# Kernel optimization log

Hardware: AMD Instinct MI355X
Metric: run time of the kernel (lower is better)

## Reference

```python
import jax, jax.numpy as jnp
import numpy as np

BETA = 0.25

def setup_inputs() -> dict:
    key = jax.random.key(0)
    k1, k2 = jax.random.split(key)
    x = jax.random.normal(k1, (32, 1024, 256), dtype=jnp.float32)
    # tf.random_uniform_initializer default range is [-0.05, 0.05)
    embedding = jax.random.uniform(k2, (256, 8192), dtype=jnp.float32, minval=-0.05, maxval=0.05)
    return {"x": x, "embedding": embedding}


def reference(x, embedding):
    # x: [B, S, D]; embedding: [D, K] (codebook stored column-wise, as in the tf module)
    D = x.shape[-1]
    flat = x.reshape(-1, D)                                   # [N, D]
    dists = (jnp.sum(flat * flat, axis=1, keepdims=True)
             - 2.0 * (flat @ embedding)
             + jnp.sum(embedding * embedding, axis=0))
    idx = jnp.argmin(dists, axis=1)                           # [N] int
    quantized = jnp.take(embedding.T, idx, axis=0).reshape(x.shape)  # gather codebook columns
    # VQ losses
    commitment = jnp.mean(jnp.square(jax.lax.stop_gradient(quantized) - x))
    codebook = jnp.mean(jnp.square(quantized - jax.lax.stop_gradient(x)))
    loss = BETA * commitment + codebook
    # straight-through estimator
    quantized_st = x + jax.lax.stop_gradient(quantized - x)
    return quantized_st, loss
```

## Files before the change

kernel.cpp:

```cpp
#include <hip/hip_runtime.h>

typedef float f4   __attribute__((ext_vector_type(4)));
typedef float f2   __attribute__((ext_vector_type(2)));
typedef _Float16 f16x8 __attribute__((ext_vector_type(8)));
typedef float f32x4  __attribute__((ext_vector_type(4)));

#define N_ROWS  32768
#define D_DIM   256
#define K_CODES 8192
#define NUM_ELEM (N_ROWS * D_DIM)
#define EPS_MARGIN 2e-3f
#define FB_CAP  8192
#define FB_RPB  8
#define RF_SLICES 16
#define N_PANELS 256
#define QTR_PANELS 64

__device__ __forceinline__ void gl2lds16(const void* g, void* l) {
    __builtin_amdgcn_global_load_lds(
        (const __attribute__((address_space(1))) unsigned int*)g,
        (__attribute__((address_space(3))) unsigned int*)l, 16, 0, 0);
}

__global__ void ee_kernel(const float* __restrict__ E, float* __restrict__ ee) {
    const int k = blockIdx.x * blockDim.x + threadIdx.x;
    double s = 0.0;
    for (int d = 0; d < D_DIM; ++d) {
        float v = E[(size_t)d * K_CODES + k];
        s += (double)v * (double)v;
    }
    ee[k] = (float)s;
}

__global__ void prep_kernel(const float* __restrict__ E, short* __restrict__ Ep) {
    const int p  = blockIdx.x;
    const int t  = threadIdx.x;
    const int c  = t & 31;
    const int gq = t >> 5;
    const int cp = p * 32;
    short* ph = Ep + (size_t)p * 8192;
    #pragma unroll
    for (int gi = 0; gi < 4; ++gi) {
        int g = gq * 4 + gi;
        f16x8 h;
        #pragma unroll
        for (int j = 0; j < 8; ++j) {
            float v = E[(size_t)(g * 8 + j) * K_CODES + cp + c];
            h[j] = (_Float16)v;
        }
        *(f16x8*)(ph + (g * 32 + c) * 8) = h;
    }
}

__global__ void trans32_kernel(const float* __restrict__ E, float* __restrict__ Et32) {
    __shared__ float tile[64][65];
    const int t  = threadIdx.x;
    const int k0 = blockIdx.x * 64, d0 = blockIdx.y * 64;
    #pragma unroll
    for (int i = 0; i < 16; ++i) {
        int dd = i * 4 + (t >> 6), kk = t & 63;
        tile[dd][kk] = E[(size_t)(d0 + dd) * K_CODES + k0 + kk];
    }
    __syncthreads();
    #pragma unroll
    for (int i = 0; i < 16; ++i) {
        int kk = i * 4 + (t >> 6), dd = t & 63;
        Et32[(size_t)(k0 + kk) * D_DIM + d0 + dd] = tile[dd][kk];
    }
}

__launch_bounds__(256, 4)
__global__ void mfma_sieve_kernel(const float* __restrict__ X,
                                  const short* __restrict__ Ep,
                                  const float* __restrict__ ee,
                                  f2* __restrict__ res_bs,
                                  int* __restrict__ res_idx) {
    __shared__ __align__(16) short Bbuf[2][8192];
    __shared__ float eebuf[2048];
    const int t    = threadIdx.x;
    const int w    = t >> 6;
    const int lane = t & 63;
    const int n    = lane & 15;
    const int quad = lane >> 4;
    const int part = blockIdx.x & 3;
    const int row0 = (blockIdx.x >> 2) * 128;
    const int rw   = row0 + w * 32;
    const int p0   = part * QTR_PANELS;

    f16x8 Ah[2][8];
    #pragma unroll
    for (int rt = 0; rt < 2; ++rt) {
        const float* xp = X + (size_t)(rw + rt * 16 + n) * D_DIM;
        #pragma unroll
        for (int ks = 0; ks < 8; ++ks) {
            int d = ks * 32 + quad * 8;
            f4 a = *(const f4*)(xp + d);
            f4 b = *(const f4*)(xp + d + 4);
            f16x8 h;
            #pragma unroll
            for (int j = 0; j < 8; ++j) {
                float x = (j < 4) ? a[j] : b[j - 4];
                h[j] = (_Float16)x;
            }
            Ah[rt][ks] = h;
        }
    }

    {
        const f4* src = (const f4*)(ee + part * 2048);
        f4* dst = (f4*)eebuf;
        dst[t * 2]     = src[t * 2];
        dst[t * 2 + 1] = src[t * 2 + 1];
    }

    float bestv[8], secv[8]; int besti[8];
    #pragma unroll
    for (int s = 0; s < 8; ++s) { bestv[s] = -1e30f; secv[s] = -1e30f; besti[s] = 0; }

    {
        const char* gp = (const char*)Ep + (size_t)p0 * 16384;
        char* lp = (char*)&Bbuf[0][0];
        #pragma unroll
        for (int i = 0; i < 4; ++i)
            gl2lds16(gp + (w * 4 + i) * 1024 + lane * 16, lp + (w * 4 + i) * 1024);
    }
    __syncthreads();

    for (int i = 0; i < QTR_PANELS; ++i) {
        const int p   = p0 + i;
        const int buf = i & 1;
        if (i + 1 < QTR_PANELS) {
            const char* gp = (const char*)Ep + (size_t)(p + 1) * 16384;
            char* lp = (char*)&Bbuf[buf ^ 1][0];
            #pragma unroll
            for (int k = 0; k < 4; ++k)
                gl2lds16(gp + (w * 4 + k) * 1024 + lane * 16, lp + (w * 4 + k) * 1024);
        }

        const short* Bh = &Bbuf[buf][0];
        const int po = i * 32;

        float eh0 = -0.5f * eebuf[po + n];
        float eh1 = -0.5f * eebuf[po + 16 + n];
        f32x4 acc[2][2];
        #pragma unroll
        for (int rt = 0; rt < 2; ++rt) {
            #pragma unroll
            for (int r = 0; r < 4; ++r) { acc[0][rt][r] = eh0; acc[1][rt][r] = eh1; }
        }

        #pragma unroll
        for (int ks = 0; ks < 8; ++ks) {
            const int g = ks * 4 + quad;
            f16x8 bh[2];
            #pragma unroll
            for (int ct = 0; ct < 2; ++ct) {
                int c = ct * 16 + n;
                bh[ct] = *(const f16x8*)(Bh + (g * 32 + c) * 8);
            }
            #pragma unroll
            for (int ct = 0; ct < 2; ++ct)
                #pragma unroll
                for (int rt = 0; rt < 2; ++rt)
                    acc[ct][rt] = __builtin_amdgcn_mfma_f32_16x16x32_f16(Ah[rt][ks], bh[ct], acc[ct][rt], 0, 0, 0);
        }

        const int cb = p * 32;
        #pragma unroll
        for (int ct = 0; ct < 2; ++ct) {
            int code = cb + ct * 16 + n;
            #pragma unroll
            for (int rt = 0; rt < 2; ++rt)
                #pragma unroll
                for (int r = 0; r < 4; ++r) {
                    float av = acc[ct][rt][r];
                    int s = rt * 4 + r;
                    float nb = fmaxf(av, bestv[s]);
                    secv[s]  = fmaxf(secv[s], fminf(av, bestv[s]));
                    besti[s] = (av > bestv[s]) ? code : besti[s];
                    bestv[s] = nb;
                }
        }
        __syncthreads();
    }

    #pragma unroll
    for (int off = 1; off < 16; off <<= 1) {
        #pragma unroll
        for (int s = 0; s < 8; ++s) {
            float ov = __shfl_xor(bestv[s], off);
            int   oi = __shfl_xor(besti[s], off);
            float os = __shfl_xor(secv[s], off);
            bool owin = (ov > bestv[s]) || (ov == bestv[s] && oi < besti[s]);
            if (owin) { secv[s] = fmaxf(os, bestv[s]); bestv[s] = ov; besti[s] = oi; }
            else      { secv[s] = fmaxf(secv[s], ov); }
        }
    }

    if (n == 0) {
        #pragma unroll
        for (int s = 0; s < 8; ++s) {
            int rl  = w * 32 + (s >> 2) * 16 + quad * 4 + (s & 3);
            int row = row0 + rl;
            f2 bs; bs[0] = -2.0f * bestv[s]; bs[1] = -2.0f * secv[s];
            res_bs[(size_t)row * 4 + part]  = bs;
            res_idx[(size_t)row * 4 + part] = besti[s];
        }
    }
}

__global__ void merge_kernel(const f2* __restrict__ res_bs, const int* __restrict__ res_idx,
                             int* __restrict__ bidx, int* __restrict__ counter,
                             int2* __restrict__ list) {
    const int row = blockIdx.x * blockDim.x + threadIdx.x;
    if (row >= N_ROWS) return;
    float gb = 1e30f, gs = 1e30f; int gi = 0;
    #pragma unroll
    for (int p = 0; p < 4; ++p) {
        f2 v  = res_bs[(size_t)row * 4 + p];
        int vi = res_idx[(size_t)row * 4 + p];
        if (v[0] < gb) { gs = fminf(gb, v[1]); gb = v[0]; gi = vi; }
        else           { gs = fminf(gs, v[0]); }
    }
    bidx[row] = gi;
    if (gs - gb <= EPS_MARGIN) {
        int pos = atomicAdd(counter, 1);
        if (pos < FB_CAP) list[pos] = make_int2(row, gi);
    }
}

__global__ void gather_kernel(const float* __restrict__ X, const float* __restrict__ Et32,
                              const int* __restrict__ bidx, float* __restrict__ out,
                              double* __restrict__ loss_sum) {
    __shared__ int bl_[128];
    const int t    = threadIdx.x;
    const int row0 = blockIdx.x * 128;
    if (t < 128) bl_[t] = bidx[row0 + t];
    __syncthreads();
    double ls = 0.0;
    const int d = t;
    #pragma unroll 4
    for (int r = 0; r < 128; ++r) {
        int code = bl_[r];
        float q  = Et32[(size_t)code * D_DIM + d];
        float x  = X[(size_t)(row0 + r) * D_DIM + d];
        float dq = q - x;
        out[(size_t)(row0 + r) * D_DIM + d] = x + dq;
        ls += (double)dq * (double)dq;
    }
    #pragma unroll
    for (int off = 32; off > 0; off >>= 1)
        ls += __shfl_down(ls, off);
    if ((t & 63) == 0) atomicAdd(loss_sum, ls);
}

__global__ void refine1_kernel(const float* __restrict__ X, const float* __restrict__ E,
                               const int* __restrict__ counter, const int2* __restrict__ list,
                               double* __restrict__ res_v, int* __restrict__ res_i) {
    __shared__ float xt[D_DIM][FB_RPB];
    __shared__ int rows_sh[FB_RPB];
    __shared__ double wbv[4][FB_RPB];
    __shared__ int    wbi[4][FB_RPB];

    int nf = *counter; if (nf > FB_CAP) nf = FB_CAP;
    const int nchunks = (nf + FB_RPB - 1) / FB_RPB;
    const int nitems  = nchunks * RF_SLICES;
    const int t = threadIdx.x;

    for (int item = blockIdx.x; item < nitems; item += gridDim.x) {
        const int rc = item / RF_SLICES;
        const int sl = item % RF_SLICES;
        __syncthreads();
        if (t < FB_RPB) {
            int e = rc * FB_RPB + t;
            int2 ent = list[(e < nf) ? e : 0];
            rows_sh[t] = ent.x;
        }
        __syncthreads();
        #pragma unroll
        for (int j = 0; j < FB_RPB; ++j)
            xt[t][j] = X[(size_t)rows_sh[j] * D_DIM + t];
        __syncthreads();

        const int k0 = sl * 512 + t * 2;
        double s0[FB_RPB], s1[FB_RPB], q0 = 0.0, q1 = 0.0;
        #pragma unroll
        for (int j = 0; j < FB_RPB; ++j) { s0[j] = 0.0; s1[j] = 0.0; }
        for (int d = 0; d < D_DIM; ++d) {
            f2 ev = *(const f2*)(E + (size_t)d * K_CODES + k0);
            double e0d = (double)ev[0], e1d = (double)ev[1];
            const f4* xp = (const f4*)(&xt[d][0]);
            f4 xa = xp[0], xb = xp[1];
            double xd[FB_RPB] = { (double)xa[0], (double)xa[1], (double)xa[2], (double)xa[3],
                                  (double)xb[0], (double)xb[1], (double)xb[2], (double)xb[3] };
            q0 += e0d * e0d; q1 += e1d * e1d;
            #pragma unroll
            for (int j = 0; j < FB_RPB; ++j) {
                s0[j] += xd[j] * e0d;
                s1[j] += xd[j] * e1d;
            }
        }
        double bv[FB_RPB]; int bi[FB_RPB];
        #pragma unroll
        for (int j = 0; j < FB_RPB; ++j) {
            double k0v = q0 - 2.0 * s0[j];
            double k1v = q1 - 2.0 * s1[j];
            bv[j] = k0v; bi[j] = k0;
            if (k1v < bv[j]) { bv[j] = k1v; bi[j] = k0 + 1; }
        }
        #pragma unroll
        for (int off = 1; off < 64; off <<= 1) {
            #pragma unroll
            for (int j = 0; j < FB_RPB; ++j) {
                double ov = __shfl_xor(bv[j], off);
                int    oi = __shfl_xor(bi[j], off);
                if (ov < bv[j] || (ov == bv[j] && oi < bi[j])) { bv[j] = ov; bi[j] = oi; }
            }
        }
        const int wave = t >> 6;
        if ((t & 63) == 0) {
            #pragma unroll
            for (int j = 0; j < FB_RPB; ++j) { wbv[wave][j] = bv[j]; wbi[wave][j] = bi[j]; }
        }
        __syncthreads();
        if (t < FB_RPB) {
            double b = wbv[0][t]; int i_ = wbi[0][t];
            #pragma unroll
            for (int wv = 1; wv < 4; ++wv) {
                double ov = wbv[wv][t]; int oi = wbi[wv][t];
                if (ov < b || (ov == b && oi < i_)) { b = ov; i_ = oi; }
            }
            int e = rc * FB_RPB + t;
            res_v[(size_t)e * RF_SLICES + sl] = b;
            res_i[(size_t)e * RF_SLICES + sl] = i_;
        }
    }
}

__global__ void patch_kernel(const float* __restrict__ X, const float* __restrict__ Et32,
                             float* __restrict__ out, double* __restrict__ loss_sum,
                             const int* __restrict__ counter, const int2* __restrict__ list,
                             const double* __restrict__ res_v, const int* __restrict__ res_i) {
    int nf = *counter; if (nf > FB_CAP) nf = FB_CAP;
    const int b = blockIdx.x;
    if (b >= nf) return;
    __shared__ int nc_sh;
    const int t = threadIdx.x;
    if (t == 0) {
        double bv = res_v[(size_t)b * RF_SLICES]; int bi = res_i[(size_t)b * RF_SLICES];
        for (int s = 1; s < RF_SLICES; ++s) {
            double v = res_v[(size_t)b * RF_SLICES + s];
            int    i = res_i[(size_t)b * RF_SLICES + s];
            if (v < bv || (v == bv && i < bi)) { bv = v; bi = i; }
        }
        nc_sh = bi;
    }
    __syncthreads();
    int2 ent = list[b];
    const int oc = ent.y, row = ent.x, nc = nc_sh;
    if (nc == oc) return;
    float x  = X[(size_t)row * D_DIM + t];
    float qn = Et32[(size_t)nc * D_DIM + t];
    float qo = Et32[(size_t)oc * D_DIM + t];
    float dqn = qn - x, dqo = qo - x;
    out[(size_t)row * D_DIM + t] = x + dqn;
    double dl = (double)dqn * dqn - (double)dqo * dqo;
    #pragma unroll
    for (int off = 32; off > 0; off >>= 1)
        dl += __shfl_down(dl, off);
    if ((t & 63) == 0) atomicAdd(loss_sum, dl);
}

__global__ void fin_kernel(const double* __restrict__ loss_sum, float* __restrict__ out) {
    double m = loss_sum[0] / (double)NUM_ELEM;
    out[NUM_ELEM] = (float)(0.25 * m + m);
}

extern "C" void kernel_launch(void* const* d_in, const int* in_sizes, int n_in,
                              void* d_out, int out_size, void* d_ws, size_t ws_size,
                              hipStream_t stream) {
    const float* X = (const float*)d_in[0];
    const float* E = (const float*)d_in[1];
    float* out = (float*)d_out;

    double* loss_sum = (double*)d_ws;
    int*    counter  = (int*)((char*)d_ws + 8);
    float*  ee       = (float*)((char*)d_ws + 1024);
    int2*   list     = (int2*)((char*)d_ws + 36864);
    double* res_v    = (double*)((char*)d_ws + 131072);
    int*    res_i    = (int*)((char*)d_ws + 1179648);
    float*  Et32     = (float*)((char*)d_ws + 1703936);
    short*  Ep       = (short*)((char*)d_ws + 10092544);
    f2*     res_bs   = (f2*)((char*)d_ws + 14286848);
    int*    res_idx  = (int*)((char*)d_ws + 15335424);
    int*    bidx     = (int*)((char*)d_ws + 19267584);

    hipMemsetAsync(d_ws, 0, 1024, stream);
    prep_kernel<<<N_PANELS, 256, 0, stream>>>(E, Ep);
    trans32_kernel<<<dim3(128, 4), 256, 0, stream>>>(E, Et32);
    ee_kernel<<<K_CODES / 256, 256, 0, stream>>>(E, ee);
    mfma_sieve_kernel<<<1024, 256, 0, stream>>>(X, Ep, ee, res_bs, res_idx);
    merge_kernel<<<N_ROWS / 256, 256, 0, stream>>>(res_bs, res_idx, bidx, counter, list);
    gather_kernel<<<N_ROWS / 128, 256, 0, stream>>>(X, Et32, bidx, out, loss_sum);
    refine1_kernel<<<2048, 256, 0, stream>>>(X, E, counter, list, res_v, res_i);
    patch_kernel<<<FB_CAP, 256, 0, stream>>>(X, Et32, out, loss_sum, counter, list,
                                             res_v, res_i);
    fin_kernel<<<1, 1, 0, stream>>>(loss_sum, out);
}
```

Baseline: 365.3 us.

## Fuse codebook prep kernels and fold merge into gather kernel

Combines the fp16 panel packing, fp32 transpose and codebook norm computation into one prep kernel that reads E once. The per-row merge of partial argmin results moves into the gather kernel, so the separate merge launch and the bidx buffer go away. The norm now accumulates in fp32 instead of fp64, which could slightly change near-tie decisions. The sieve kernel's launch-bounds occupancy hint also drops from 4 to 2 blocks per CU, which gives it more registers but lowers occupancy.

```diff
diff --git a/kernel.cpp b/kernel.cpp
--- a/kernel.cpp
+++ b/kernel.cpp
@@ -22,54 +22,43 @@
         (__attribute__((address_space(3))) unsigned int*)l, 16, 0, 0);
 }
 
-__global__ void ee_kernel(const float* __restrict__ E, float* __restrict__ ee) {
-    const int k = blockIdx.x * blockDim.x + threadIdx.x;
-    double s = 0.0;
-    for (int d = 0; d < D_DIM; ++d) {
-        float v = E[(size_t)d * K_CODES + k];
-        s += (double)v * (double)v;
-    }
-    ee[k] = (float)s;
-}
-
-__global__ void prep_kernel(const float* __restrict__ E, short* __restrict__ Ep) {
+__global__ void prep_kernel(const float* __restrict__ E, short* __restrict__ Ep,
+                            float* __restrict__ Et32, float* __restrict__ ee) {
+    __shared__ float eepart[8][32];
     const int p  = blockIdx.x;
     const int t  = threadIdx.x;
     const int c  = t & 31;
     const int gq = t >> 5;
     const int cp = p * 32;
     short* ph = Ep + (size_t)p * 8192;
+    float ss = 0.0f;
     #pragma unroll
     for (int gi = 0; gi < 4; ++gi) {
         int g = gq * 4 + gi;
         f16x8 h;
+        f4 av, bv;
         #pragma unroll
         for (int j = 0; j < 8; ++j) {
             float v = E[(size_t)(g * 8 + j) * K_CODES + cp + c];
             h[j] = (_Float16)v;
+            ss += v * v;
+            if (j < 4) av[j] = v; else bv[j - 4] = v;
         }
         *(f16x8*)(ph + (g * 32 + c) * 8) = h;
-    }
-}
-
-__global__ void trans32_kernel(const float* __restrict__ E, float* __restrict__ Et32) {
-    __shared__ float tile[64][65];
-    const int t  = threadIdx.x;
-    const int k0 = blockIdx.x * 64, d0 = blockIdx.y * 64;
-    #pragma unroll
-    for (int i = 0; i < 16; ++i) {
-        int dd = i * 4 + (t >> 6), kk = t & 63;
-        tile[dd][kk] = E[(size_t)(d0 + dd) * K_CODES + k0 + kk];
-    }
+        *(f4*)(Et32 + (size_t)(cp + c) * D_DIM + g * 8)     = av;
+        *(f4*)(Et32 + (size_t)(cp + c) * D_DIM + g * 8 + 4) = bv;
+    }
+    eepart[gq][c] = ss;
     __syncthreads();
-    #pragma unroll
-    for (int i = 0; i < 16; ++i) {
-        int kk = i * 4 + (t >> 6), dd = t & 63;
-        Et32[(size_t)(k0 + kk) * D_DIM + d0 + dd] = tile[dd][kk];
-    }
-}
-
-__launch_bounds__(256, 4)
+    if (t < 32) {
+        float s = 0.0f;
+        #pragma unroll
+        for (int q = 0; q < 8; ++q) s += eepart[q][t];
+        ee[cp + t] = s;
+    }
+}
+
+__launch_bounds__(256, 2)
 __global__ void mfma_sieve_kernel(const float* __restrict__ X,
                                   const short* __restrict__ Ep,
                                   const float* __restrict__ ee,
@@ -209,33 +198,29 @@
     }
 }
 
-__global__ void merge_kernel(const f2* __restrict__ res_bs, const int* __restrict__ res_idx,
-                             int* __restrict__ bidx, int* __restrict__ counter,
-                             int2* __restrict__ list) {
-    const int row = blockIdx.x * blockDim.x + threadIdx.x;
-    if (row >= N_ROWS) return;
-    float gb = 1e30f, gs = 1e30f; int gi = 0;
-    #pragma unroll
-    for (int p = 0; p < 4; ++p) {
-        f2 v  = res_bs[(size_t)row * 4 + p];
-        int vi = res_idx[(size_t)row * 4 + p];
-        if (v[0] < gb) { gs = fminf(gb, v[1]); gb = v[0]; gi = vi; }
-        else           { gs = fminf(gs, v[0]); }
-    }
-    bidx[row] = gi;
-    if (gs - gb <= EPS_MARGIN) {
-        int pos = atomicAdd(counter, 1);
-        if (pos < FB_CAP) list[pos] = make_int2(row, gi);
-    }
-}
-
 __global__ void gather_kernel(const float* __restrict__ X, const float* __restrict__ Et32,
-                              const int* __restrict__ bidx, float* __restrict__ out,
-                              double* __restrict__ loss_sum) {
+                              const f2* __restrict__ res_bs, const int* __restrict__ res_idx,
+                              int* __restrict__ counter, int2* __restrict__ list,
+                              float* __restrict__ out, double* __restrict__ loss_sum) {
     __shared__ int bl_[128];
     const int t    = threadIdx.x;
     const int row0 = blockIdx.x * 128;
-    if (t < 128) bl_[t] = bidx[row0 + t];
+    if (t < 128) {
+        const int row = row0 + t;
+        float gb = 1e30f, gs = 1e30f; int gi = 0;
+        #pragma unroll
+        for (int p = 0; p < 4; ++p) {
+            f2 v  = res_bs[(size_t)row * 4 + p];
+            int vi = res_idx[(size_t)row * 4 + p];
+            if (v[0] < gb) { gs = fminf(gb, v[1]); gb = v[0]; gi = vi; }
+            else           { gs = fminf(gs, v[0]); }
+        }
+        bl_[t] = gi;
+        if (gs - gb <= EPS_MARGIN) {
+            int pos = atomicAdd(counter, 1);
+            if (pos < FB_CAP) list[pos] = make_int2(row, gi);
+        }
+    }
     __syncthreads();
     double ls = 0.0;
     const int d = t;
@@ -393,15 +378,12 @@
     short*  Ep       = (short*)((char*)d_ws + 10092544);
     f2*     res_bs   = (f2*)((char*)d_ws + 14286848);
     int*    res_idx  = (int*)((char*)d_ws + 15335424);
-    int*    bidx     = (int*)((char*)d_ws + 19267584);
 
     hipMemsetAsync(d_ws, 0, 1024, stream);
-    prep_kernel<<<N_PANELS, 256, 0, stream>>>(E, Ep);
-    trans32_kernel<<<dim3(128, 4), 256, 0, stream>>>(E, Et32);
-    ee_kernel<<<K_CODES / 256, 256, 0, stream>>>(E, ee);
+    prep_kernel<<<N_PANELS, 256, 0, stream>>>(E, Ep, Et32, ee);
     mfma_sieve_kernel<<<1024, 256, 0, stream>>>(X, Ep, ee, res_bs, res_idx);
-    merge_kernel<<<N_ROWS / 256, 256, 0, stream>>>(res_bs, res_idx, bidx, counter, list);
-    gather_kernel<<<N_ROWS / 128, 256, 0, stream>>>(X, Et32, bidx, out, loss_sum);
+    gather_kernel<<<N_ROWS / 128, 256, 0, stream>>>(X, Et32, res_bs, res_idx,
+                                                    counter, list, out, loss_sum);
     refine1_kernel<<<2048, 256, 0, stream>>>(X, E, counter, list, res_v, res_i);
     patch_kernel<<<FB_CAP, 256, 0, stream>>>(X, Et32, out, loss_sum, counter, list,
                                              res_v, res_i);
```

Measured after the change: 364.2 us. No clear change (-0.3%).
